# Optimization experiments

Hardware: AMD Instinct MI355X
Metric: run time of the kernel (lower is better)

## Reference

```python
import jax, jax.numpy as jnp
import numpy as np

N_NODES = 100000
N_EDGES = 1600000
N_GRAPHS = 256
D_IN = 128
D_HID = 128
D_OUT = 64


def graph_conv(x, src, dst, W_rel, b_rel, W_root):
    # PyG GraphConv: out = lin_rel(mean_{j->i} x_j) + lin_root(x)
    msgs = jax.ops.segment_sum(x[src], dst, num_segments=N_NODES)  # [N, d]
    deg = jax.ops.segment_sum(jnp.ones((src.shape[0],), x.dtype), dst, num_segments=N_NODES)
    agg = msgs / jnp.maximum(deg, 1.0)[:, None]
    return agg @ W_rel + b_rel + x @ W_root


def setup_inputs() -> dict:
    key = jax.random.key(0)
    ks = jax.random.split(key, 12)
    x = jax.random.normal(ks[0], (N_NODES, D_IN), dtype=jnp.float32)
    edge_index = jax.random.randint(ks[1], (2, N_EDGES), 0, N_NODES, dtype=jnp.int64)
    batch = jnp.sort(jax.random.randint(ks[2], (N_NODES,), 0, N_GRAPHS, dtype=jnp.int64))
    def lin(k, fan_in, fan_out):
        bound = 1.0 / np.sqrt(fan_in)
        return jax.random.uniform(k, (fan_in, fan_out), jnp.float32, -bound, bound)
    inp = {
        "x": x, "edge_index": edge_index, "batch": batch,
        "W1_rel": lin(ks[3], D_IN, D_HID), "b1_rel": jnp.zeros((D_HID,), jnp.float32), "W1_root": lin(ks[4], D_IN, D_HID),
        "W2_rel": lin(ks[5], D_HID, D_HID), "b2_rel": jnp.zeros((D_HID,), jnp.float32), "W2_root": lin(ks[6], D_HID, D_HID),
        "W3_rel": lin(ks[7], D_HID, D_HID), "b3_rel": jnp.zeros((D_HID,), jnp.float32), "W3_root": lin(ks[8], D_HID, D_HID),
        "Wl": lin(ks[9], D_HID, D_OUT), "bl": jnp.zeros((D_OUT,), jnp.float32),
    }
    return inp


def reference(x, edge_index, batch, W1_rel, b1_rel, W1_root, W2_rel, b2_rel, W2_root,
              W3_rel, b3_rel, W3_root, Wl, bl):
    src, dst = edge_index[0], edge_index[1]
    h = jax.nn.relu(graph_conv(x, src, dst, W1_rel, b1_rel, W1_root))
    h = jax.nn.relu(graph_conv(h, src, dst, W2_rel, b2_rel, W2_root))
    h = graph_conv(h, src, dst, W3_rel, b3_rel, W3_root)
    # global mean pool over graphs
    sums = jax.ops.segment_sum(h, batch, num_segments=N_GRAPHS)          # [G, d]
    cnts = jax.ops.segment_sum(jnp.ones((h.shape[0],), h.dtype), batch, num_segments=N_GRAPHS)
    pooled = sums / jnp.maximum(cnts, 1.0)[:, None]
    # dropout is identity at inference
    return pooled @ Wl + bl  # [G, D_OUT]
```

## Files before the change

### kernel.cpp

```cpp
#include <hip/hip_runtime.h>
#include <hip/hip_bf16.h>

#define N_NODES  100000
#define N_EDGES  1600000
#define N_GRAPHS 256
#define DCH      128
#define DOUT     64
#define NB       391
#define PADB     512
#define SLACK    4608
#define CHUNK    4096
#define PCH      64

typedef short v8s __attribute__((ext_vector_type(8)));
typedef float v4f __attribute__((ext_vector_type(4)));

static __device__ __forceinline__ float bf2f(unsigned short u) {
    unsigned int x = ((unsigned int)u) << 16;
    return __builtin_bit_cast(float, x);
}
static __device__ __forceinline__ unsigned short f2bf(float f) {
    unsigned int x = __builtin_bit_cast(unsigned int, f);
    unsigned int r = (x + 0x7fffu + ((x >> 16) & 1u)) >> 16;
    return (unsigned short)r;
}
static __device__ __forceinline__ int clampi(int v, int lo, int hi) {
    return v < lo ? lo : (v > hi ? hi : v);
}

__global__ void cvt_kernel(const float* __restrict__ in, unsigned short* __restrict__ out) {
    size_t i = ((size_t)blockIdx.x * blockDim.x + threadIdx.x) * 4;
    if (i + 3 < (size_t)N_NODES * DCH) {
        float4 f = *reinterpret_cast<const float4*>(in + i);
        uint2 o;
        o.x = ((unsigned)f2bf(f.y) << 16) | (unsigned)f2bf(f.x);
        o.y = ((unsigned)f2bf(f.w) << 16) | (unsigned)f2bf(f.z);
        *reinterpret_cast<uint2*>(out + i) = o;
    }
}

__global__ void __launch_bounds__(256) binA_kernel(const int* __restrict__ src, const int* __restrict__ dst,
                                                   int* __restrict__ gcur, uint2* __restrict__ region) {
    __shared__ uint2 stage[CHUNK];
    __shared__ int hcnt[PADB], hcnt2[PADB], hoff[PADB], garr[PADB];
    __shared__ int s2[256];
    int tid = threadIdx.x;
    int e0  = blockIdx.x * CHUNK;
    int nedge = N_EDGES - e0; if (nedge > CHUNK) nedge = CHUNK;

    for (int b = tid; b < PADB; b += 256) { hcnt[b] = 0; hcnt2[b] = 0; }
    __syncthreads();

    int es[16], ed[16];
    #pragma unroll
    for (int j = 0; j < 16; j++) {
        int e = e0 + j * 256 + tid;
        if (e < N_EDGES) {
            es[j] = clampi(src[e], 0, N_NODES - 1);
            ed[j] = clampi(dst[e], 0, N_NODES - 1);
            atomicAdd(&hcnt[ed[j] >> 8], 1);
        } else { es[j] = -1; ed[j] = 0; }
    }
    __syncthreads();

    int v0 = hcnt[2 * tid], v1 = hcnt[2 * tid + 1];
    s2[tid] = v0 + v1; __syncthreads();
    for (int off = 1; off < 256; off <<= 1) {
        int x = (tid >= off) ? s2[tid - off] : 0;
        __syncthreads();
        s2[tid] += x;
        __syncthreads();
    }
    int excl = s2[tid] - (v0 + v1);
    hoff[2 * tid] = excl; hoff[2 * tid + 1] = excl + v0;
    __syncthreads();

    for (int b = tid; b < NB; b += 256) {
        int c = hcnt[b];
        garr[b] = b * SLACK + ((c > 0) ? atomicAdd(&gcur[b], c) : 0);
    }
    __syncthreads();

    #pragma unroll
    for (int j = 0; j < 16; j++) {
        if (es[j] >= 0) {
            int b = ed[j] >> 8;
            int pos = atomicAdd(&hcnt2[b], 1) + hoff[b];
            stage[pos] = (uint2){(unsigned)es[j], (unsigned)ed[j]};
        }
    }
    __syncthreads();

    for (int i = tid; i < nedge; i += 256) {
        uint2 en = stage[i];
        int b = (int)(en.y >> 8);
        int gpos = garr[b] + (i - hoff[b]);
        if (gpos < (b + 1) * SLACK) region[gpos] = en;
    }
}

__global__ void __launch_bounds__(256) binFinish_kernel(const uint2* __restrict__ region, const int* __restrict__ gcur,
                                                        int* __restrict__ rowptr, int* __restrict__ csr) {
    __shared__ int h[256], sc[256], cur[256], s2[256], hoff[PADB];
    int b = blockIdx.x, tid = threadIdx.x;
    int c0 = gcur[2 * tid];     if (c0 > SLACK) c0 = SLACK;
    int c1 = gcur[2 * tid + 1]; if (c1 > SLACK) c1 = SLACK;
    s2[tid] = c0 + c1;
    h[tid] = 0;
    __syncthreads();
    for (int off = 1; off < 256; off <<= 1) {
        int x = (tid >= off) ? s2[tid - off] : 0;
        __syncthreads();
        s2[tid] += x;
        __syncthreads();
    }
    int excl = s2[tid] - (c0 + c1);
    hoff[2 * tid] = excl; hoff[2 * tid + 1] = excl + c0;
    __syncthreads();
    if (b == 0 && tid == 255) rowptr[N_NODES] = hoff[511];
    int base = hoff[b];
    int size = gcur[b]; if (size > SLACK) size = SLACK;
    int node0 = b * 256;
    for (int j = tid; j < size; j += 256) {
        unsigned loc = region[b * SLACK + j].y - (unsigned)node0;
        if (loc < 256u) atomicAdd(&h[loc], 1);
    }
    __syncthreads();
    int v = h[tid]; sc[tid] = v; __syncthreads();
    for (int off = 1; off < 256; off <<= 1) {
        int x = (tid >= off) ? sc[tid - off] : 0;
        __syncthreads();
        sc[tid] += x;
        __syncthreads();
    }
    int myptr = base + sc[tid] - v;
    int node = node0 + tid;
    if (node < N_NODES) rowptr[node] = myptr;
    cur[tid] = myptr;
    __syncthreads();
    for (int j = tid; j < size; j += 256) {
        uint2 en = region[b * SLACK + j];
        unsigned loc = en.y - (unsigned)node0;
        if (loc < 256u) {
            int p = atomicAdd(&cur[loc], 1);
            if (p >= 0 && p < N_EDGES) csr[p] = (int)en.x;
        }
    }
}

__global__ void wfrag_kernel(const float* __restrict__ W1rel, const float* __restrict__ W1root,
                             const float* __restrict__ W2rel, const float* __restrict__ W2root,
                             const float* __restrict__ W3rel, const float* __restrict__ W3root,
                             unsigned short* __restrict__ frag) {
    int gid = blockIdx.x * blockDim.x + threadIdx.x;
    if (gid >= 3 * 8 * 8 * 64) return;
    int lane = gid & 63;
    int nt   = (gid >> 6) & 7;
    int kt   = (gid >> 9) & 7;
    int L    = gid >> 12;
    const float* rel  = (L == 0) ? W1rel  : (L == 1) ? W2rel  : W3rel;
    const float* root = (L == 0) ? W1root : (L == 1) ? W2root : W3root;
    int n  = nt * 16 + (lane & 15);
    int k0 = kt * 32 + (lane >> 4) * 8;
    unsigned short o[8];
    #pragma unroll
    for (int j = 0; j < 8; j++) {
        int k = k0 + j;
        float w = (k < 128) ? rel[k * 128 + n] : root[(k - 128) * 128 + n];
        o[j] = f2bf(w);
    }
    uint4 u;
    u.x = (unsigned)o[0] | ((unsigned)o[1] << 16);
    u.y = (unsigned)o[2] | ((unsigned)o[3] << 16);
    u.z = (unsigned)o[4] | ((unsigned)o[5] << 16);
    u.w = (unsigned)o[6] | ((unsigned)o[7] << 16);
    *reinterpret_cast<uint4*>(frag + (size_t)gid * 8) = u;
}

__global__ void agg_kernel(const unsigned short* __restrict__ hin, const int* __restrict__ rowptr,
                           const int* __restrict__ csr, unsigned short* __restrict__ agg) {
    int wave = threadIdx.x >> 6;
    int lane = threadIdx.x & 63;
    int node = blockIdx.x * 4 + wave;
    if (node >= N_NODES) return;
    int r0 = rowptr[node], r1 = rowptr[node + 1];
    int l16 = lane & 15;
    float a0 = 0.f, a1 = 0.f;
    for (int c = r0; c < r1; c += 16) {
        int m = r1 - c; if (m > 16) m = 16;
        int idx = csr[c + (l16 < m ? l16 : 0)];
        #pragma unroll
        for (int j = 0; j < 16; j++) {
            int s = __shfl(idx, j);
            unsigned int v = *reinterpret_cast<const unsigned int*>(hin + (size_t)s * DCH + lane * 2);
            float w = (j < m) ? 1.0f : 0.0f;
            a0 = fmaf(w, bf2f((unsigned short)(v & 0xffffu)), a0);
            a1 = fmaf(w, bf2f((unsigned short)(v >> 16)), a1);
        }
    }
    int deg = r1 - r0;
    float inv = 1.0f / (float)(deg > 1 ? deg : 1);
    a0 *= inv; a1 *= inv;
    unsigned int o = ((unsigned int)f2bf(a1) << 16) | (unsigned int)f2bf(a0);
    *reinterpret_cast<unsigned int*>(agg + (size_t)node * DCH + lane * 2) = o;
}

__global__ void gemm_kernel(const unsigned short* agg, const unsigned short* __restrict__ root,
                            const unsigned short* __restrict__ frag, const float* __restrict__ bias,
                            unsigned short* hout, int relu) {
    int wave = threadIdx.x >> 6;
    int lane = threadIdx.x & 63;
    int quad = lane >> 4;
    int ml   = lane & 15;
    int base = blockIdx.x * 128 + wave * 32;
    int r0 = clampi(base + ml, 0, N_NODES - 1);
    int r1 = clampi(base + 16 + ml, 0, N_NODES - 1);
    v4f acc[2][8];
    #pragma unroll
    for (int h = 0; h < 2; h++)
        #pragma unroll
        for (int nt = 0; nt < 8; nt++) acc[h][nt] = (v4f){0.f, 0.f, 0.f, 0.f};
    #pragma unroll
    for (int kt = 0; kt < 8; kt++) {
        const unsigned short* asrc = (kt < 4) ? agg : root;
        int ak = (kt & 3) * 32 + quad * 8;
        v8s a0 = *reinterpret_cast<const v8s*>(asrc + (size_t)r0 * DCH + ak);
        v8s a1 = *reinterpret_cast<const v8s*>(asrc + (size_t)r1 * DCH + ak);
        #pragma unroll
        for (int nt = 0; nt < 8; nt++) {
            v8s b = *reinterpret_cast<const v8s*>(frag + (((size_t)(kt * 8 + nt)) * 64 + lane) * 8);
            acc[0][nt] = __builtin_amdgcn_mfma_f32_16x16x32_bf16(a0, b, acc[0][nt], 0, 0, 0);
            acc[1][nt] = __builtin_amdgcn_mfma_f32_16x16x32_bf16(a1, b, acc[1][nt], 0, 0, 0);
        }
    }
    #pragma unroll
    for (int h = 0; h < 2; h++) {
        int mbase = base + h * 16 + quad * 4;
        #pragma unroll
        for (int nt = 0; nt < 8; nt++) {
            int n = nt * 16 + ml;
            float bv = bias[n];
            #pragma unroll
            for (int r = 0; r < 4; r++) {
                int row = mbase + r;
                if (row < N_NODES) {
                    float v = acc[h][nt][r] + bv;
                    if (relu) v = fmaxf(v, 0.f);
                    hout[(size_t)row * DCH + n] = f2bf(v);
                }
            }
        }
    }
}

__global__ void __launch_bounds__(128) pool_kernel(const unsigned short* __restrict__ h,
                                                   const int* __restrict__ batch,
                                                   float* __restrict__ psum) {
    int c  = threadIdx.x;
    int n0 = blockIdx.x * PCH;
    int n1 = n0 + PCH < N_NODES ? n0 + PCH : N_NODES;
    if (n0 >= n1) return;
    int cur = clampi(batch[n0], 0, N_GRAPHS - 1);
    float acc = 0.f;
    for (int n = n0; n < n1; n++) {
        int g = clampi(batch[n], 0, N_GRAPHS - 1);
        if (g != cur) {
            atomicAdd(&psum[cur * DCH + c], acc);
            acc = 0.f; cur = g;
        }
        acc += bf2f(h[(size_t)n * DCH + c]);
    }
    atomicAdd(&psum[cur * DCH + c], acc);
}

static __device__ __forceinline__ int lowerb(const int* __restrict__ a, int n, int key) {
    int lo = 0, hi = n;
    while (lo < hi) { int mid = (lo + hi) >> 1; if (a[mid] < key) lo = mid + 1; else hi = mid; }
    return lo;
}

__global__ void __launch_bounds__(64) final_kernel(const float* __restrict__ psum,
                                                   const int* __restrict__ batch,
                                                   const float* __restrict__ Wl, const float* __restrict__ bl,
                                                   float* __restrict__ out) {
    __shared__ float ps[DCH];
    __shared__ int bounds[2];
    int g = blockIdx.x, tid = threadIdx.x;
    if (tid == 0) {
        bounds[0] = lowerb(batch, N_NODES, g);
        bounds[1] = lowerb(batch, N_NODES, g + 1);
    }
    __syncthreads();
    int cnt = bounds[1] - bounds[0];
    float inv = 1.0f / (float)(cnt > 1 ? cnt : 1);
    ps[tid] = psum[g * DCH + tid] * inv;
    ps[tid + 64] = psum[g * DCH + tid + 64] * inv;
    __syncthreads();
    float o = 0.f;
    #pragma unroll 4
    for (int c = 0; c < DCH; c++) o += ps[c] * Wl[c * DOUT + tid];
    out[g * DOUT + tid] = o + bl[tid];
}

extern "C" void kernel_launch(void* const* d_in, const int* in_sizes, int n_in,
                              void* d_out, int out_size, void* d_ws, size_t ws_size,
                              hipStream_t stream) {
    const float* x     = (const float*)d_in[0];
    const int*   edge  = (const int*)d_in[1];
    const int*   src   = edge;
    const int*   dst   = edge + N_EDGES;
    const int*   batch = (const int*)d_in[2];
    const float* W1rel  = (const float*)d_in[3];
    const float* b1     = (const float*)d_in[4];
    const float* W1root = (const float*)d_in[5];
    const float* W2rel  = (const float*)d_in[6];
    const float* b2     = (const float*)d_in[7];
    const float* W2root = (const float*)d_in[8];
    const float* W3rel  = (const float*)d_in[9];
    const float* b3     = (const float*)d_in[10];
    const float* W3root = (const float*)d_in[11];
    const float* Wl     = (const float*)d_in[12];
    const float* bl     = (const float*)d_in[13];
    float* out = (float*)d_out;

    char* ws = (char*)d_ws;
    size_t off = 0;
    auto carve = [&](size_t bytes) -> void* {
        void* p = ws + off;
        off += (bytes + 255) & ~(size_t)255;
        return p;
    };
    int*            rowptr  = (int*)carve((size_t)(N_NODES + 1) * 4);
    int*            csr     = (int*)carve((size_t)N_EDGES * 4);
    int*            gcur    = (int*)carve((size_t)PADB * 4 + (size_t)N_GRAPHS * DCH * 4);
    float*          psum    = (float*)(gcur + PADB);
    unsigned short* frag    = (unsigned short*)carve((size_t)3 * 8 * 8 * 64 * 8 * 2);
    unsigned short* B1      = (unsigned short*)carve((size_t)N_NODES * DCH * 2);
    unsigned short* B2      = (unsigned short*)carve((size_t)N_NODES * DCH * 2);
    uint2*          region  = (uint2*)B1;

    hipMemsetAsync(gcur, 0, (size_t)PADB * 4 + (size_t)N_GRAPHS * DCH * 4, stream);

    binA_kernel<<<(N_EDGES + CHUNK - 1) / CHUNK, 256, 0, stream>>>(src, dst, gcur, region);
    binFinish_kernel<<<NB, 256, 0, stream>>>(region, gcur, rowptr, csr);
    cvt_kernel<<<(N_NODES * DCH / 4 + 255) / 256, 256, 0, stream>>>(x, B2);
    wfrag_kernel<<<(3 * 8 * 8 * 64 + 255) / 256, 256, 0, stream>>>(W1rel, W1root, W2rel, W2root, W3rel, W3root, frag);

    const int aggGrid  = (N_NODES + 3) / 4;
    const int gemmGrid = (N_NODES + 127) / 128;

    agg_kernel<<<aggGrid, 256, 0, stream>>>(B2, rowptr, csr, B1);
    gemm_kernel<<<gemmGrid, 256, 0, stream>>>(B1, B2, frag, b1, B1, 1);
    agg_kernel<<<aggGrid, 256, 0, stream>>>(B1, rowptr, csr, B2);
    gemm_kernel<<<gemmGrid, 256, 0, stream>>>(B2, B1, frag + 32768, b2, B2, 1);
    agg_kernel<<<aggGrid, 256, 0, stream>>>(B2, rowptr, csr, B1);
    gemm_kernel<<<gemmGrid, 256, 0, stream>>>(B1, B2, frag + 65536, b3, B1, 0);

    pool_kernel<<<(N_NODES + PCH - 1) / PCH, 128, 0, stream>>>(B1, batch, psum);
    final_kernel<<<N_GRAPHS, 64, 0, stream>>>(psum, batch, Wl, bl, out);
}
```

Before: 447.1 us.

## Fuse neighbor aggregation and GEMM into one per-layer kernel via LDS tile

Replaces the separate aggregation and MFMA GEMM kernels with one layer kernel. Each 64-thread block aggregates 32 nodes' mean neighbor features into a swizzled LDS tile, then runs the rel+root GEMM straight from LDS and global. This removes the round trip of the aggregated matrix through HBM and half the launches. Out-of-range edge slots now point at a zeroed padding row, so the per-edge masking multiply becomes a plain add. The cost is a single wave per block that serially gathers 32 nodes, which lowers parallelism and latency hiding during the gather phase.

Result: faster. 423.8 us (-5.2%).

```diff
diff --git a/kernel.cpp b/kernel.cpp
--- a/kernel.cpp
+++ b/kernel.cpp
@@ -177,60 +177,66 @@
     *reinterpret_cast<uint4*>(frag + (size_t)gid * 8) = u;
 }
 
-__global__ void agg_kernel(const unsigned short* __restrict__ hin, const int* __restrict__ rowptr,
-                           const int* __restrict__ csr, unsigned short* __restrict__ agg) {
-    int wave = threadIdx.x >> 6;
-    int lane = threadIdx.x & 63;
-    int node = blockIdx.x * 4 + wave;
-    if (node >= N_NODES) return;
-    int r0 = rowptr[node], r1 = rowptr[node + 1];
-    int l16 = lane & 15;
-    float a0 = 0.f, a1 = 0.f;
-    for (int c = r0; c < r1; c += 16) {
-        int m = r1 - c; if (m > 16) m = 16;
-        int idx = csr[c + (l16 < m ? l16 : 0)];
-        #pragma unroll
-        for (int j = 0; j < 16; j++) {
-            int s = __shfl(idx, j);
-            unsigned int v = *reinterpret_cast<const unsigned int*>(hin + (size_t)s * DCH + lane * 2);
-            float w = (j < m) ? 1.0f : 0.0f;
-            a0 = fmaf(w, bf2f((unsigned short)(v & 0xffffu)), a0);
-            a1 = fmaf(w, bf2f((unsigned short)(v >> 16)), a1);
-        }
-    }
-    int deg = r1 - r0;
-    float inv = 1.0f / (float)(deg > 1 ? deg : 1);
-    a0 *= inv; a1 *= inv;
-    unsigned int o = ((unsigned int)f2bf(a1) << 16) | (unsigned int)f2bf(a0);
-    *reinterpret_cast<unsigned int*>(agg + (size_t)node * DCH + lane * 2) = o;
-}
-
-__global__ void gemm_kernel(const unsigned short* agg, const unsigned short* __restrict__ root,
-                            const unsigned short* __restrict__ frag, const float* __restrict__ bias,
-                            unsigned short* hout, int relu) {
-    int wave = threadIdx.x >> 6;
-    int lane = threadIdx.x & 63;
-    int quad = lane >> 4;
-    int ml   = lane & 15;
-    int base = blockIdx.x * 128 + wave * 32;
-    int r0 = clampi(base + ml, 0, N_NODES - 1);
-    int r1 = clampi(base + 16 + ml, 0, N_NODES - 1);
+__global__ void __launch_bounds__(64, 4) layer_kernel(
+    const unsigned short* __restrict__ hin,
+    const int* __restrict__ rowptr, const int* __restrict__ csr,
+    const unsigned short* __restrict__ frag, const float* __restrict__ bias,
+    unsigned short* __restrict__ hout, int relu)
+{
+    __shared__ __attribute__((aligned(16))) unsigned short As[32 * DCH];
+    const int lane = threadIdx.x & 63;
+    const int l16  = lane & 15;
+    const int quad = lane >> 4;
+    const int base = blockIdx.x * 32;
+
+    int rp = rowptr[base + (lane < 33 ? lane : 32)];
+
+    char* Asb = reinterpret_cast<char*>(As);
+
+    for (int i = 0; i < 32; i++) {
+        int r0 = __builtin_amdgcn_readlane(rp, i);
+        int r1 = __builtin_amdgcn_readlane(rp, i + 1);
+        float a0 = 0.f, a1 = 0.f;
+        for (int c = r0; c < r1; c += 16) {
+            int e = c + l16;
+            int idx = (e < r1) ? csr[e] : N_NODES;
+            #pragma unroll
+            for (int j = 0; j < 16; j++) {
+                int s = __builtin_amdgcn_readlane(idx, j);
+                unsigned v = *reinterpret_cast<const unsigned*>(hin + (size_t)s * DCH + lane * 2);
+                a0 += bf2f((unsigned short)(v & 0xffffu));
+                a1 += bf2f((unsigned short)(v >> 16));
+            }
+        }
+        int deg = r1 - r0;
+        float inv = 1.0f / (float)(deg > 1 ? deg : 1);
+        unsigned o = ((unsigned)f2bf(a1 * inv) << 16) | (unsigned)f2bf(a0 * inv);
+        *reinterpret_cast<unsigned*>(Asb + i * 256 + ((lane * 4) ^ ((i & 7) << 4))) = o;
+    }
+
     v4f acc[2][8];
     #pragma unroll
     for (int h = 0; h < 2; h++)
         #pragma unroll
         for (int nt = 0; nt < 8; nt++) acc[h][nt] = (v4f){0.f, 0.f, 0.f, 0.f};
+
     #pragma unroll
     for (int kt = 0; kt < 8; kt++) {
-        const unsigned short* asrc = (kt < 4) ? agg : root;
-        int ak = (kt & 3) * 32 + quad * 8;
-        v8s a0 = *reinterpret_cast<const v8s*>(asrc + (size_t)r0 * DCH + ak);
-        v8s a1 = *reinterpret_cast<const v8s*>(asrc + (size_t)r1 * DCH + ak);
+        v8s a0v, a1v;
+        if (kt < 4) {
+            int co = (kt * 64 + quad * 16) ^ ((l16 & 7) << 4);
+            a0v = *reinterpret_cast<const v8s*>(Asb + l16 * 256 + co);
+            a1v = *reinterpret_cast<const v8s*>(Asb + (16 + l16) * 256 + co);
+        } else {
+            int ak = (kt - 4) * 32 + quad * 8;
+            a0v = *reinterpret_cast<const v8s*>(hin + (size_t)(base + l16) * DCH + ak);
+            a1v = *reinterpret_cast<const v8s*>(hin + (size_t)(base + 16 + l16) * DCH + ak);
+        }
         #pragma unroll
         for (int nt = 0; nt < 8; nt++) {
             v8s b = *reinterpret_cast<const v8s*>(frag + (((size_t)(kt * 8 + nt)) * 64 + lane) * 8);
-            acc[0][nt] = __builtin_amdgcn_mfma_f32_16x16x32_bf16(a0, b, acc[0][nt], 0, 0, 0);
-            acc[1][nt] = __builtin_amdgcn_mfma_f32_16x16x32_bf16(a1, b, acc[1][nt], 0, 0, 0);
+            acc[0][nt] = __builtin_amdgcn_mfma_f32_16x16x32_bf16(a0v, b, acc[0][nt], 0, 0, 0);
+            acc[1][nt] = __builtin_amdgcn_mfma_f32_16x16x32_bf16(a1v, b, acc[1][nt], 0, 0, 0);
         }
     }
     #pragma unroll
@@ -238,16 +244,13 @@
         int mbase = base + h * 16 + quad * 4;
         #pragma unroll
         for (int nt = 0; nt < 8; nt++) {
-            int n = nt * 16 + ml;
+            int n = nt * 16 + l16;
             float bv = bias[n];
             #pragma unroll
             for (int r = 0; r < 4; r++) {
-                int row = mbase + r;
-                if (row < N_NODES) {
-                    float v = acc[h][nt][r] + bv;
-                    if (relu) v = fmaxf(v, 0.f);
-                    hout[(size_t)row * DCH + n] = f2bf(v);
-                }
+                float v = acc[h][nt][r] + bv;
+                if (relu) v = fmaxf(v, 0.f);
+                hout[(size_t)(mbase + r) * DCH + n] = f2bf(v);
             }
         }
     }
@@ -331,30 +334,28 @@
         return p;
     };
     int*            rowptr  = (int*)carve((size_t)(N_NODES + 1) * 4);
-    int*            csr     = (int*)carve((size_t)N_EDGES * 4);
+    int*            csr     = (int*)carve((size_t)(N_EDGES + 16) * 4);
     int*            gcur    = (int*)carve((size_t)PADB * 4 + (size_t)N_GRAPHS * DCH * 4);
     float*          psum    = (float*)(gcur + PADB);
     unsigned short* frag    = (unsigned short*)carve((size_t)3 * 8 * 8 * 64 * 8 * 2);
-    unsigned short* B1      = (unsigned short*)carve((size_t)N_NODES * DCH * 2);
-    unsigned short* B2      = (unsigned short*)carve((size_t)N_NODES * DCH * 2);
+    unsigned short* B1      = (unsigned short*)carve((size_t)(N_NODES + 1) * DCH * 2);
+    unsigned short* B2      = (unsigned short*)carve((size_t)(N_NODES + 1) * DCH * 2);
     uint2*          region  = (uint2*)B1;
 
     hipMemsetAsync(gcur, 0, (size_t)PADB * 4 + (size_t)N_GRAPHS * DCH * 4, stream);
+    hipMemsetAsync(B1 + (size_t)N_NODES * DCH, 0, (size_t)DCH * 2, stream);
+    hipMemsetAsync(B2 + (size_t)N_NODES * DCH, 0, (size_t)DCH * 2, stream);
 
     binA_kernel<<<(N_EDGES + CHUNK - 1) / CHUNK, 256, 0, stream>>>(src, dst, gcur, region);
     binFinish_kernel<<<NB, 256, 0, stream>>>(region, gcur, rowptr, csr);
     cvt_kernel<<<(N_NODES * DCH / 4 + 255) / 256, 256, 0, stream>>>(x, B2);
     wfrag_kernel<<<(3 * 8 * 8 * 64 + 255) / 256, 256, 0, stream>>>(W1rel, W1root, W2rel, W2root, W3rel, W3root, frag);
 
-    const int aggGrid  = (N_NODES + 3) / 4;
-    const int gemmGrid = (N_NODES + 127) / 128;
-
-    agg_kernel<<<aggGrid, 256, 0, stream>>>(B2, rowptr, csr, B1);
-    gemm_kernel<<<gemmGrid, 256, 0, stream>>>(B1, B2, frag, b1, B1, 1);
-    agg_kernel<<<aggGrid, 256, 0, stream>>>(B1, rowptr, csr, B2);
-    gemm_kernel<<<gemmGrid, 256, 0, stream>>>(B2, B1, frag + 32768, b2, B2, 1);
-    agg_kernel<<<aggGrid, 256, 0, stream>>>(B2, rowptr, csr, B1);
-    gemm_kernel<<<gemmGrid, 256, 0, stream>>>(B1, B2, frag + 65536, b3, B1, 0);
+    const int layerGrid = N_NODES / 32;
+
+    layer_kernel<<<layerGrid, 64, 0, stream>>>(B2, rowptr, csr, frag,         b1, B1, 1);
+    layer_kernel<<<layerGrid, 64, 0, stream>>>(B1, rowptr, csr, frag + 32768, b2, B2, 1);
+    layer_kernel<<<layerGrid, 64, 0, stream>>>(B2, rowptr, csr, frag + 65536, b3, B1, 0);
 
     pool_kernel<<<(N_NODES + PCH - 1) / PCH, 128, 0, stream>>>(B1, batch, psum);
     final_kernel<<<N_GRAPHS, 64, 0, stream>>>(psum, batch, Wl, bl, out);
```
